# Optimization experiments

Measured on AMD Instinct MI355X. Metric: run time of the kernel, lower is better.

The kernel has to match this reference:

```python
import jax, jax.numpy as jnp
import numpy as np

N_USERS = 100000
N_ITEMS = 50000
D = 64          # latent_dimension
BU = 1024       # batch of user ids
BI = 4096       # batch of item ids
L = 50          # nonzeros per user row of implicit feedback (padded)


def _xavier(key, n, d):
    std = float(np.sqrt(2.0 / (n + d)))
    return jax.random.normal(key, (n, d), dtype=jnp.float32) * std


def setup_inputs() -> dict:
    key = jax.random.key(0)
    ks = jax.random.split(key, 8)
    user_ids = jax.random.randint(ks[0], (BU,), 0, N_USERS)
    item_ids = jax.random.randint(ks[1], (BI,), 0, N_ITEMS)
    # padded sparse rows of implicit_feedback_normalized for the batch users
    fb_indices = jax.random.randint(ks[2], (BU, L), 0, N_ITEMS)
    v = jax.random.uniform(ks[3], (BU, L), dtype=jnp.float32)
    fb_values = v / (jnp.sum(v, axis=-1, keepdims=True) + 1e-8)  # rows sum to 1
    return {
        "user_ids": user_ids,
        "item_ids": item_ids,
        "fb_indices": fb_indices,
        "fb_values": fb_values,
        "user_weight": _xavier(ks[4], N_USERS, D),
        "user_bias": jnp.zeros((N_USERS, 1), dtype=jnp.float32),
        "item_weight": _xavier(ks[5], N_ITEMS, D),
        "item_bias": jnp.zeros((N_ITEMS, 1), dtype=jnp.float32),
        "bias": jnp.zeros((1,), dtype=jnp.float32),
        "item_rating_effect_weight": _xavier(ks[6], N_ITEMS, D),
    }


def reference(user_ids, item_ids, fb_indices, fb_values,
              user_weight, user_bias, item_weight, item_bias, bias,
              item_rating_effect_weight):
    uw = user_weight[user_ids]            # [BU, D]
    ub = user_bias[user_ids]              # [BU, 1]
    iw = item_weight[item_ids]            # [BI, D]
    ib = item_bias[item_ids]              # [BI, 1]
    # base PMF rating: uw @ iw.T + biases
    rating = uw @ iw.T + ub + ib.T + bias  # [BU, BI]
    # sparse row-weighted sum over item_rating_effect_weight (segment reduce)
    gathered = item_rating_effect_weight[fb_indices]          # [BU, L, D]
    offset = jnp.einsum('bl,bld->bd', fb_values, gathered)    # [BU, D]
    rating = rating + offset @ iw.T
    return rating
```

## Files before the change

### kernel.cpp

```cpp
#include <hip/hip_runtime.h>
#include <hip/hip_bf16.h>

#define D 64
#define BU 1024
#define BI 4096
#define L 50

typedef __attribute__((ext_vector_type(4))) float f32x4;
typedef __attribute__((ext_vector_type(8))) short bf16x8;

__device__ __forceinline__ ushort f2bf(float x) {
    union { float f; unsigned u; } v; v.f = x;
    unsigned r = v.u + 0x7fff + ((v.u >> 16) & 1);
    return (ushort)(r >> 16);
}

__global__ __launch_bounds__(256) void k_eff(
    const int* __restrict__ user_ids, const int* __restrict__ fb_idx,
    const float* __restrict__ fb_val, const float* __restrict__ uw,
    const float* __restrict__ ub, const float* __restrict__ We,
    ushort* __restrict__ eff, float* __restrict__ ubg) {
    const int u = blockIdx.x * 4 + (threadIdx.x >> 6);
    const int d = threadIdx.x & 63;
    const int uid = user_ids[u];
    float acc = uw[uid * D + d];
    const int*   __restrict__ ip = fb_idx + u * L;
    const float* __restrict__ vp = fb_val + u * L;
    #pragma unroll 10
    for (int l = 0; l < L; ++l)
        acc = fmaf(vp[l], We[ip[l] * D + d], acc);
    eff[u * D + d] = f2bf(acc);
    if (d == 0) ubg[u] = ub[uid];
}

__global__ __launch_bounds__(256) void k_items(
    const int* __restrict__ item_ids, const float* __restrict__ iw,
    const float* __restrict__ ib, ushort* __restrict__ iwg,
    float* __restrict__ ibg) {
    const int n = blockIdx.x * 4 + (threadIdx.x >> 6);
    const int d = threadIdx.x & 63;
    const int iid = item_ids[n];
    iwg[n * D + d] = f2bf(iw[iid * D + d]);
    if (d == 0) ibg[n] = ib[iid];
}

__global__ __launch_bounds__(256) void k_gemm(
    const ushort* __restrict__ eff, const ushort* __restrict__ iwg,
    const float* __restrict__ ubg, const float* __restrict__ ibg,
    const float* __restrict__ bias, float* __restrict__ out) {
    const int lane = threadIdx.x & 63;
    const int wave = threadIdx.x >> 6;
    const int m0 = blockIdx.y * 16;
    const int n0 = blockIdx.x * 256 + wave * 64;
    const int lr = lane & 15;
    const int g  = lane >> 4;

    const bf16x8 a0 = *(const bf16x8*)(eff + (m0 + lr) * D + g * 8);
    const bf16x8 a1 = *(const bf16x8*)(eff + (m0 + lr) * D + 32 + g * 8);

    f32x4 acc[4];
    #pragma unroll
    for (int c = 0; c < 4; ++c) {
        acc[c] = (f32x4){0.f, 0.f, 0.f, 0.f};
        const int col = n0 + c * 16 + lr;
        const bf16x8 b0 = *(const bf16x8*)(iwg + col * D + g * 8);
        const bf16x8 b1 = *(const bf16x8*)(iwg + col * D + 32 + g * 8);
        acc[c] = __builtin_amdgcn_mfma_f32_16x16x32_bf16(a0, b0, acc[c], 0, 0, 0);
        acc[c] = __builtin_amdgcn_mfma_f32_16x16x32_bf16(a1, b1, acc[c], 0, 0, 0);
    }

    const float bb = bias[0];
    float ubr[4];
    #pragma unroll
    for (int r = 0; r < 4; ++r) ubr[r] = ubg[m0 + g * 4 + r];

    #pragma unroll
    for (int c = 0; c < 4; ++c) {
        const int col = n0 + c * 16 + lr;
        const float ibc = ibg[col] + bb;
        #pragma unroll
        for (int r = 0; r < 4; ++r)
            out[(size_t)(m0 + g * 4 + r) * BI + col] = acc[c][r] + ubr[r] + ibc;
    }
}

extern "C" void kernel_launch(void* const* d_in, const int* in_sizes, int n_in,
                              void* d_out, int out_size, void* d_ws, size_t ws_size,
                              hipStream_t stream) {
    const int*   user_ids = (const int*)  d_in[0];
    const int*   item_ids = (const int*)  d_in[1];
    const int*   fb_idx   = (const int*)  d_in[2];
    const float* fb_val   = (const float*)d_in[3];
    const float* uw       = (const float*)d_in[4];
    const float* ub       = (const float*)d_in[5];
    const float* iw       = (const float*)d_in[6];
    const float* ib       = (const float*)d_in[7];
    const float* bias     = (const float*)d_in[8];
    const float* We       = (const float*)d_in[9];

    char* ws = (char*)d_ws;
    ushort* eff = (ushort*)(ws);
    ushort* iwg = (ushort*)(ws + 131072);
    float*  ubg = (float*)(ws + 131072 + 524288);
    float*  ibg = (float*)(ws + 131072 + 524288 + 4096);

    float* out = (float*)d_out;

    k_eff<<<BU / 4, 256, 0, stream>>>(user_ids, fb_idx, fb_val, uw, ub, We, eff, ubg);
    k_items<<<BI / 4, 256, 0, stream>>>(item_ids, iw, ib, iwg, ibg);
    k_gemm<<<dim3(BI / 256, BU / 16), 256, 0, stream>>>(eff, iwg, ubg, ibg, bias, out);
}
```

Baseline: 20.84 us.

## Fuse gather, item prep and GEMM into one cooperative kernel with grid sync

```diff
diff --git a/kernel.cpp b/kernel.cpp
--- a/kernel.cpp
+++ b/kernel.cpp
@@ -1,5 +1,8 @@
 #include <hip/hip_runtime.h>
 #include <hip/hip_bf16.h>
+#include <hip/hip_cooperative_groups.h>
+
+namespace cg = cooperative_groups;
 
 #define D 64
 #define BU 1024
@@ -15,72 +18,92 @@
     return (ushort)(r >> 16);
 }
 
-__global__ __launch_bounds__(256) void k_eff(
-    const int* __restrict__ user_ids, const int* __restrict__ fb_idx,
-    const float* __restrict__ fb_val, const float* __restrict__ uw,
-    const float* __restrict__ ub, const float* __restrict__ We,
-    ushort* __restrict__ eff, float* __restrict__ ubg) {
-    const int u = blockIdx.x * 4 + (threadIdx.x >> 6);
-    const int d = threadIdx.x & 63;
-    const int uid = user_ids[u];
-    float acc = uw[uid * D + d];
-    const int*   __restrict__ ip = fb_idx + u * L;
-    const float* __restrict__ vp = fb_val + u * L;
-    #pragma unroll 10
-    for (int l = 0; l < L; ++l)
-        acc = fmaf(vp[l], We[ip[l] * D + d], acc);
-    eff[u * D + d] = f2bf(acc);
-    if (d == 0) ubg[u] = ub[uid];
-}
+__global__ __launch_bounds__(256) void k_fused(
+    const int* __restrict__ user_ids, const int* __restrict__ item_ids,
+    const int* __restrict__ fb_idx, const float* __restrict__ fb_val,
+    const float* __restrict__ uw, const float* __restrict__ ub,
+    const float* __restrict__ iw, const float* __restrict__ ib,
+    const float* __restrict__ bias, const float* __restrict__ We,
+    ushort* __restrict__ eff, ushort* __restrict__ iwg,
+    float* __restrict__ ubg, float* __restrict__ ibg,
+    float* __restrict__ out) {
+    const int t = threadIdx.x;
+    const int b = blockIdx.x;
+    const int wave = t >> 6;
+    const int lane = t & 63;
 
-__global__ __launch_bounds__(256) void k_items(
-    const int* __restrict__ item_ids, const float* __restrict__ iw,
-    const float* __restrict__ ib, ushort* __restrict__ iwg,
-    float* __restrict__ ibg) {
-    const int n = blockIdx.x * 4 + (threadIdx.x >> 6);
-    const int d = threadIdx.x & 63;
-    const int iid = item_ids[n];
-    iwg[n * D + d] = f2bf(iw[iid * D + d]);
-    if (d == 0) ibg[n] = ib[iid];
-}
+    {
+        const int u = b * 4 + wave;
+        const int uid = user_ids[u];
+        float acc = uw[uid * D + lane];
+        const int*   __restrict__ ip = fb_idx + u * L;
+        const float* __restrict__ vp = fb_val + u * L;
+        #pragma unroll 10
+        for (int l = 0; l < L; ++l)
+            acc = fmaf(vp[l], We[ip[l] * D + lane], acc);
+        eff[u * D + lane] = f2bf(acc);
+        if (lane == 0) ubg[u] = ub[uid];
+    }
 
-__global__ __launch_bounds__(256) void k_gemm(
-    const ushort* __restrict__ eff, const ushort* __restrict__ iwg,
-    const float* __restrict__ ubg, const float* __restrict__ ibg,
-    const float* __restrict__ bias, float* __restrict__ out) {
-    const int lane = threadIdx.x & 63;
-    const int wave = threadIdx.x >> 6;
-    const int m0 = blockIdx.y * 16;
-    const int n0 = blockIdx.x * 256 + wave * 64;
+    {
+        const int it = b * 16 + (t >> 4);
+        const int iid = item_ids[it];
+        const int d4 = (t & 15) * 4;
+        const float4 v = *(const float4*)(iw + (size_t)iid * D + d4);
+        ushort4 o;
+        o.x = f2bf(v.x); o.y = f2bf(v.y); o.z = f2bf(v.z); o.w = f2bf(v.w);
+        *(ushort4*)(iwg + it * D + d4) = o;
+        if (t < 16) ibg[b * 16 + t] = ib[item_ids[b * 16 + t]];
+    }
+
+    cg::this_grid().sync();
+
+    const int m0 = (b >> 4) * 64;
+    const int n0 = (b & 15) * 256 + wave * 64;
     const int lr = lane & 15;
     const int g  = lane >> 4;
 
-    const bf16x8 a0 = *(const bf16x8*)(eff + (m0 + lr) * D + g * 8);
-    const bf16x8 a1 = *(const bf16x8*)(eff + (m0 + lr) * D + 32 + g * 8);
-
-    f32x4 acc[4];
+    bf16x8 a0[4], a1[4], b0[4], b1[4];
     #pragma unroll
-    for (int c = 0; c < 4; ++c) {
-        acc[c] = (f32x4){0.f, 0.f, 0.f, 0.f};
-        const int col = n0 + c * 16 + lr;
-        const bf16x8 b0 = *(const bf16x8*)(iwg + col * D + g * 8);
-        const bf16x8 b1 = *(const bf16x8*)(iwg + col * D + 32 + g * 8);
-        acc[c] = __builtin_amdgcn_mfma_f32_16x16x32_bf16(a0, b0, acc[c], 0, 0, 0);
-        acc[c] = __builtin_amdgcn_mfma_f32_16x16x32_bf16(a1, b1, acc[c], 0, 0, 0);
+    for (int mt = 0; mt < 4; ++mt) {
+        const int row = m0 + mt * 16 + lr;
+        a0[mt] = *(const bf16x8*)(eff + row * D + g * 8);
+        a1[mt] = *(const bf16x8*)(eff + row * D + 32 + g * 8);
+    }
+    #pragma unroll
+    for (int ct = 0; ct < 4; ++ct) {
+        const int col = n0 + ct * 16 + lr;
+        b0[ct] = *(const bf16x8*)(iwg + col * D + g * 8);
+        b1[ct] = *(const bf16x8*)(iwg + col * D + 32 + g * 8);
     }
 
+    f32x4 acc[4][4];
+    #pragma unroll
+    for (int mt = 0; mt < 4; ++mt)
+        #pragma unroll
+        for (int ct = 0; ct < 4; ++ct) {
+            acc[mt][ct] = (f32x4){0.f, 0.f, 0.f, 0.f};
+            acc[mt][ct] = __builtin_amdgcn_mfma_f32_16x16x32_bf16(a0[mt], b0[ct], acc[mt][ct], 0, 0, 0);
+            acc[mt][ct] = __builtin_amdgcn_mfma_f32_16x16x32_bf16(a1[mt], b1[ct], acc[mt][ct], 0, 0, 0);
+        }
+
     const float bb = bias[0];
-    float ubr[4];
+    float ibc[4];
     #pragma unroll
-    for (int r = 0; r < 4; ++r) ubr[r] = ubg[m0 + g * 4 + r];
+    for (int ct = 0; ct < 4; ++ct) ibc[ct] = ibg[n0 + ct * 16 + lr] + bb;
 
     #pragma unroll
-    for (int c = 0; c < 4; ++c) {
-        const int col = n0 + c * 16 + lr;
-        const float ibc = ibg[col] + bb;
+    for (int mt = 0; mt < 4; ++mt) {
+        float ubr[4];
         #pragma unroll
-        for (int r = 0; r < 4; ++r)
-            out[(size_t)(m0 + g * 4 + r) * BI + col] = acc[c][r] + ubr[r] + ibc;
+        for (int r = 0; r < 4; ++r) ubr[r] = ubg[m0 + mt * 16 + g * 4 + r];
+        #pragma unroll
+        for (int ct = 0; ct < 4; ++ct) {
+            const int col = n0 + ct * 16 + lr;
+            #pragma unroll
+            for (int r = 0; r < 4; ++r)
+                out[(size_t)(m0 + mt * 16 + g * 4 + r) * BI + col] = acc[mt][ct][r] + ubr[r] + ibc[ct];
+        }
     }
 }
 
@@ -103,10 +126,10 @@
     ushort* iwg = (ushort*)(ws + 131072);
     float*  ubg = (float*)(ws + 131072 + 524288);
     float*  ibg = (float*)(ws + 131072 + 524288 + 4096);
+    float*  out = (float*)d_out;
 
-    float* out = (float*)d_out;
-
-    k_eff<<<BU / 4, 256, 0, stream>>>(user_ids, fb_idx, fb_val, uw, ub, We, eff, ubg);
-    k_items<<<BI / 4, 256, 0, stream>>>(item_ids, iw, ib, iwg, ibg);
-    k_gemm<<<dim3(BI / 256, BU / 16), 256, 0, stream>>>(eff, iwg, ubg, ibg, bias, out);
+    void* args[] = { (void*)&user_ids, (void*)&item_ids, (void*)&fb_idx, (void*)&fb_val,
+                     (void*)&uw, (void*)&ub, (void*)&iw, (void*)&ib, (void*)&bias, (void*)&We,
+                     (void*)&eff, (void*)&iwg, (void*)&ubg, (void*)&ibg, (void*)&out };
+    hipLaunchCooperativeKernel((const void*)k_fused, dim3(256), dim3(256), args, 0, stream);
 }
```

After: 58.88 us. 183% more time.

## Fuse user-effect and item-gather prep kernels and split feedback reduction across waves

Applied to the files above, without the earlier changes.

```diff
diff --git a/kernel.cpp b/kernel.cpp
--- a/kernel.cpp
+++ b/kernel.cpp
@@ -15,33 +15,58 @@
     return (ushort)(r >> 16);
 }
 
-__global__ __launch_bounds__(256) void k_eff(
-    const int* __restrict__ user_ids, const int* __restrict__ fb_idx,
-    const float* __restrict__ fb_val, const float* __restrict__ uw,
-    const float* __restrict__ ub, const float* __restrict__ We,
-    ushort* __restrict__ eff, float* __restrict__ ubg) {
-    const int u = blockIdx.x * 4 + (threadIdx.x >> 6);
-    const int d = threadIdx.x & 63;
-    const int uid = user_ids[u];
-    float acc = uw[uid * D + d];
-    const int*   __restrict__ ip = fb_idx + u * L;
-    const float* __restrict__ vp = fb_val + u * L;
-    #pragma unroll 10
-    for (int l = 0; l < L; ++l)
-        acc = fmaf(vp[l], We[ip[l] * D + d], acc);
-    eff[u * D + d] = f2bf(acc);
-    if (d == 0) ubg[u] = ub[uid];
-}
+__global__ __launch_bounds__(256) void k_prep(
+    const int* __restrict__ user_ids, const int* __restrict__ item_ids,
+    const int* __restrict__ fb_idx, const float* __restrict__ fb_val,
+    const float* __restrict__ uw, const float* __restrict__ ub,
+    const float* __restrict__ iw, const float* __restrict__ ib,
+    const float* __restrict__ We,
+    ushort* __restrict__ eff, ushort* __restrict__ iwg,
+    float* __restrict__ ubg, float* __restrict__ ibg) {
+    const int b = blockIdx.x;
+    const int t = threadIdx.x;
 
-__global__ __launch_bounds__(256) void k_items(
-    const int* __restrict__ item_ids, const float* __restrict__ iw,
-    const float* __restrict__ ib, ushort* __restrict__ iwg,
-    float* __restrict__ ibg) {
-    const int n = blockIdx.x * 4 + (threadIdx.x >> 6);
-    const int d = threadIdx.x & 63;
-    const int iid = item_ids[n];
-    iwg[n * D + d] = f2bf(iw[iid * D + d]);
-    if (d == 0) ibg[n] = ib[iid];
+    if (b < BU) {
+        __shared__ float s_part[4][D];
+        const int wave = t >> 6;
+        const int lane = t & 63;
+        const int u = b;
+        const int lo = wave * 13;
+        float acc = 0.f;
+        #pragma unroll
+        for (int j = 0; j < 13; ++j) {
+            const int l = lo + j;
+            if (l < L) {
+                const int   ix = fb_idx[u * L + l];
+                const float v  = fb_val[u * L + l];
+                acc = fmaf(v, We[(size_t)ix * D + lane], acc);
+            }
+        }
+        s_part[wave][lane] = acc;
+        __syncthreads();
+        if (wave == 0) {
+            const int uid = user_ids[u];
+            const float r = uw[(size_t)uid * D + lane]
+                          + s_part[0][lane] + s_part[1][lane]
+                          + s_part[2][lane] + s_part[3][lane];
+            eff[u * D + lane] = f2bf(r);
+            if (lane == 0) ubg[u] = ub[uid];
+        }
+    } else {
+        const int base = (b - BU) * 32;
+        const int row  = base + (t >> 3);
+        const int seg  = (t & 7) * 8;
+        const int iid  = item_ids[row];
+        const float4 f0 = *(const float4*)(iw + (size_t)iid * D + seg);
+        const float4 f1 = *(const float4*)(iw + (size_t)iid * D + seg + 4);
+        bf16x8 o;
+        o[0] = (short)f2bf(f0.x); o[1] = (short)f2bf(f0.y);
+        o[2] = (short)f2bf(f0.z); o[3] = (short)f2bf(f0.w);
+        o[4] = (short)f2bf(f1.x); o[5] = (short)f2bf(f1.y);
+        o[6] = (short)f2bf(f1.z); o[7] = (short)f2bf(f1.w);
+        *(bf16x8*)(iwg + row * D + seg) = o;
+        if (t < 32) ibg[base + t] = ib[item_ids[base + t]];
+    }
 }
 
 __global__ __launch_bounds__(256) void k_gemm(
@@ -103,10 +128,9 @@
     ushort* iwg = (ushort*)(ws + 131072);
     float*  ubg = (float*)(ws + 131072 + 524288);
     float*  ibg = (float*)(ws + 131072 + 524288 + 4096);
+    float*  out = (float*)d_out;
 
-    float* out = (float*)d_out;
-
-    k_eff<<<BU / 4, 256, 0, stream>>>(user_ids, fb_idx, fb_val, uw, ub, We, eff, ubg);
-    k_items<<<BI / 4, 256, 0, stream>>>(item_ids, iw, ib, iwg, ibg);
+    k_prep<<<BU + BI / 32, 256, 0, stream>>>(user_ids, item_ids, fb_idx, fb_val,
+                                             uw, ub, iw, ib, We, eff, iwg, ubg, ibg);
     k_gemm<<<dim3(BI / 256, BU / 16), 256, 0, stream>>>(eff, iwg, ubg, ibg, bias, out);
 }
```

Result: no change. 20.56 us (median of 2 runs) (-1.4%).
